# Kernel tuning notes

Hardware: AMD Instinct MI355X
Metric: run time of the kernel (lower is better)

Reference implementation:

```python
import math
import jax, jax.numpy as jnp
import numpy as np

N_HEAD = 4
D_MODEL = 96
BS, N_TOK = 32, 512
A2LEN = 150          # a2len % 16 != 0 so padn > 0 (asserted in torch code)
DST_MXLEN = 32


def setup_inputs() -> dict:
    key = jax.random.key(0)
    k1, k2, k3, k4, k5, k6 = jax.random.split(key, 6)
    x = jax.random.normal(k1, (BS, N_TOK, D_MODEL), dtype=jnp.float32)
    # LinearM: w is [outdim, indim+1], last column is the bias, zeroed at init
    wqv_w = 0.02 * jax.random.normal(k2, (3 * D_MODEL, D_MODEL + 1), dtype=jnp.float32)
    wqv_w = wqv_w.at[:, -1].set(0.0)
    fanout_w = 0.02 * jax.random.normal(k3, (D_MODEL, D_MODEL + 1), dtype=jnp.float32)
    fanout_w = fanout_w.at[:, -1].set(0.0)

    def make_coo(k):
        # COO triples [dst, src, dst_cnt]; every dst has DST_MXLEN sources
        dst = jnp.repeat(jnp.arange(N_TOK), DST_MXLEN)
        src = jax.random.randint(k, (N_TOK * DST_MXLEN,), 0, N_TOK)
        cnt = jnp.tile(jnp.arange(DST_MXLEN), N_TOK)
        return jnp.stack([dst, src, cnt], axis=1).astype(jnp.int32)

    coo0 = make_coo(k4)
    coo1 = make_coo(k5)
    a2a = jnp.sort(jax.random.permutation(k6, N_TOK)[:A2LEN]).astype(jnp.int32)
    return {"x": x, "wqv_w": wqv_w, "fanout_w": fanout_w,
            "coo0": coo0, "coo1": coo1, "a2a": a2a, "dst_mxlen": DST_MXLEN}


def _linm(w, x):
    # LinearM: einsum('oi,bhi->bho') + bias column
    return jnp.einsum('oi,bti->bto', w[:, :-1], x) + w[:, -1]


def _l1attn_sparse(v, q, k, coo, dst_mxlen):
    # l1attn_sparse_cuda.L1AttnSparse: per-(dst,src) L1 scores scattered into a
    # [n_tok, dst_mxlen] ragged table (pad = -1e12), softmax over the fan-in slot.
    bs, n_tok, h, w = q.shape
    dst, src, cnt = coo[:, 0], coo[:, 1], coo[:, 2]
    scale = 1.0 / math.sqrt(w)
    ww = -jnp.sum(jnp.abs(q[:, dst] - k[:, src]), axis=-1) * scale    # [bs, cl, h]
    attn = jnp.full((bs, n_tok, dst_mxlen, h), -1e12, dtype=q.dtype)
    attn = attn.at[:, dst, cnt, :].set(ww)
    attn_sm = jax.nn.softmax(attn, axis=2)
    vw = jnp.zeros((bs, n_tok, dst_mxlen, h, w), dtype=q.dtype)
    vw = vw.at[:, dst, cnt, :, :].set(v[:, src])                      # gather by src
    return jnp.einsum('bdrh,bdrhw->bdhw', attn_sm, vw)


def _forward(x, wqv_w, fanout_w, coo0, coo1, a2a, dst_mxlen):
    bs, n_tok, width = x.shape
    h = N_HEAD
    y = _linm(wqv_w, x)
    q, k, v = jnp.split(y, 3, axis=-1)

    # --- dense all-to-all L1 attention on tokens a2a, channels 72:96 (h*6) ---
    a2len = a2a.shape[0]
    q1 = q[:, a2a, 72:].reshape(bs, a2len, h, 6)
    k1 = k[:, a2a, 72:].reshape(bs, a2len, h, 6)
    v1 = v[:, a2a, 72:].reshape(bs, a2len, h, 6)
    padl = (a2len + 15) // 16 * 16
    q2 = jnp.pad(q1, ((0, 0), (0, padl - a2len), (0, 0), (0, 0)))
    k2 = jnp.pad(k1, ((0, 0), (0, padl - a2len), (0, 0), (0, 0)))
    scale = 1.0 / math.sqrt(6)
    # l1attn_cuda.L1Attn: a[b, s, d, h] = -scale * sum_w |q[b,d,h,w] - k[b,s,h,w]|
    a = -jnp.sum(jnp.abs(q2[:, None, :, :, :] - k2[:, :, None, :, :]), axis=-1) * scale
    a = a[:, :a2len + 1, :a2len + 1, :]   # keep one zero-score pad row (attention sink)
    a = jax.nn.softmax(a, axis=1)         # softmax over src dim
    a = a[:, :a2len, :a2len, :]
    b1 = jnp.einsum('bsdh,bshw->bdhw', a, v1)
    b2 = jnp.zeros((bs, n_tok, h, 6), dtype=x.dtype).at[:, a2a].set(b1)
    dense = b2.reshape(bs, n_tok, h * 6)

    # --- two sparse COO L1-attention groups: channels 32:52 and 52:72 (h*5) ---
    sparse_out = []
    for i, coo in enumerate((coo0, coo1)):
        sta = 32 + 20 * i
        q1 = q[:, :, sta:sta + 20].reshape(bs, n_tok, h, 5)
        k1 = k[:, :, sta:sta + 20].reshape(bs, n_tok, h, 5)
        v1 = v[:, :, sta:sta + 20].reshape(bs, n_tok, h, 5)
        sparse_out.append(_l1attn_sparse(v1, q1, k1, coo, dst_mxlen).reshape(bs, n_tok, h * 5))

    # channels 0:32 are never written -> zeros
    b = jnp.concatenate([jnp.zeros((bs, n_tok, 32), dtype=x.dtype),
                         sparse_out[0], sparse_out[1], dense], axis=-1)
    yb = b * jax.nn.sigmoid(1.702 * b)    # QuickGELU
    return x + _linm(fanout_w, yb)


def reference(x, wqv_w, fanout_w, coo0, coo1, a2a, dst_mxlen):
    return _forward(x, wqv_w, fanout_w, coo0, coo1, a2a, dst_mxlen)
```

## Files before the change

### kernel.cpp

```cpp
#include <hip/hip_runtime.h>
#include <hip/hip_bf16.h>
#include <math.h>

#define BS   32
#define T    512
#define BT   (BS * T)
#define D    96
#define H    4
#define MX   32
#define A2MAX 160

#define QKV_TOK  8
#define FUSE_TOK 8
#define DT       32

__global__ void transpose_kernel(const float* __restrict__ wqv,
                                 const float* __restrict__ fw,
                                 float* __restrict__ WT, float* __restrict__ FWT) {
    int idx = blockIdx.x * blockDim.x + threadIdx.x;
    if (idx < 97 * 192) {
        const int i = idx / 192, oc = idx - 192 * i;
        const int p = oc >> 6, c = oc & 63;
        WT[idx] = wqv[(p * 96 + 32 + c) * 97 + i];
    }
    idx -= 97 * 192;
    if (idx >= 0 && idx < 65 * 96) {
        const int i = idx / 96, o = idx - 96 * i;
        FWT[idx] = fw[o * 97 + 32 + i];
    }
}

__global__ void qkv_kernel(const float* __restrict__ x, const float* __restrict__ WT,
                           float* __restrict__ Q, float* __restrict__ K,
                           float* __restrict__ V) {
    const int tid  = threadIdx.x;
    const int base = blockIdx.x * QKV_TOK;
    __shared__ float xs[QKV_TOK * D];
    #pragma unroll
    for (int j = 0; j < 4; ++j) xs[tid + 192 * j] = x[base * D + tid + 192 * j];
    __syncthreads();
    float acc[QKV_TOK];
    const float bias = WT[96 * 192 + tid];
    #pragma unroll
    for (int j = 0; j < QKV_TOK; ++j) acc[j] = bias;
    #pragma unroll 4
    for (int i = 0; i < D; ++i) {
        const float wv = WT[i * 192 + tid];
        #pragma unroll
        for (int j = 0; j < QKV_TOK; ++j) acc[j] += wv * xs[j * D + i];
    }
    const int part = tid >> 6, c = tid & 63;
    float* out = (part == 0) ? Q : (part == 1 ? K : V);
    #pragma unroll
    for (int j = 0; j < QKV_TOK; ++j) out[(base + j) * 64 + c] = acc[j];
}

__global__ void scatter_kernel(const int* __restrict__ coo0,
                               const int* __restrict__ coo1,
                               int* __restrict__ srcs, int nedges) {
    const int id = blockIdx.x * blockDim.x + threadIdx.x;
    if (id >= 2 * nedges) return;
    const int ci = id / nedges;
    const int e  = id - ci * nedges;
    const int* row = (ci == 0 ? coo0 : coo1) + e * 3;
    const int dst = row[0], src = row[1], cnt = row[2];
    if (dst >= 0 && dst < T && cnt >= 0 && cnt < MX)
        srcs[(ci * T + dst) * MX + cnt] = src;
}

__global__ void sparse_kernel(const float* __restrict__ Q, const float* __restrict__ K,
                              const float* __restrict__ V, const int* __restrict__ srcs,
                              float* __restrict__ B) {
    const int b   = blockIdx.y;
    const int ci  = blockIdx.x >> 2, h = blockIdx.x & 3;
    const int base = 20 * ci + h * 5;
    const int tid  = threadIdx.x;
    __shared__ float ks[T * 8];
    __shared__ float vs[T * 8];
    for (int i = tid; i < T * 5; i += 256) {
        const int s = i / 5, w = i - 5 * s;
        const int g = (b * T + s) * 64 + base + w;
        ks[s * 8 + w] = K[g];
        vs[s * 8 + w] = V[g];
    }
    __syncthreads();
    const float iscale = 0.4472135954999579f;
    for (int t = tid; t < T; t += 256) {
        const int* sp   = srcs + (ci * T + t) * MX;
        const float* qp = Q + (b * T + t) * 64 + base;
        const float q0 = qp[0], q1 = qp[1], q2 = qp[2], q3 = qp[3], q4 = qp[4];
        float l = 0.f, o0 = 0.f, o1 = 0.f, o2 = 0.f, o3 = 0.f, o4 = 0.f;
        #pragma unroll 4
        for (int c = 0; c < MX; ++c) {
            const int s = sp[c];
            if (s < 0) continue;
            const float4 k4 = *(const float4*)&ks[s * 8];
            const float  k5 = ks[s * 8 + 4];
            const float sum = fabsf(q0 - k4.x) + fabsf(q1 - k4.y) +
                              fabsf(q2 - k4.z) + fabsf(q3 - k4.w) + fabsf(q4 - k5);
            const float e = __expf(-sum * iscale);
            const float4 v4 = *(const float4*)&vs[s * 8];
            const float  v5 = vs[s * 8 + 4];
            l  += e;
            o0 += e * v4.x; o1 += e * v4.y; o2 += e * v4.z;
            o3 += e * v4.w; o4 += e * v5;
        }
        const float inv = (l > 0.f) ? 1.f / l : 0.f;
        float* bp = B + (b * T + t) * 96 + 32 + base;
        bp[0] = o0 * inv; bp[1] = o1 * inv; bp[2] = o2 * inv;
        bp[3] = o3 * inv; bp[4] = o4 * inv;
    }
}

__global__ void dense_kernel(const float* __restrict__ Q, const float* __restrict__ K,
                             const float* __restrict__ V, const int* __restrict__ a2a,
                             int a2len, int extra, float* __restrict__ B) {
    const int b   = blockIdx.y;
    const int d0  = blockIdx.x * DT;
    const int tid = threadIdx.x;
    __shared__ int   rows[A2MAX];
    __shared__ float ks[A2MAX * 32];
    __shared__ float vs[A2MAX * 32];
    for (int i = tid; i < a2len; i += 128) rows[i] = a2a[i];
    __syncthreads();
    for (int i = tid; i < a2len * 24; i += 128) {
        const int s = i / 24, w = i - 24 * s;
        const int hh = w / 6, ww = w - 6 * hh;
        const int g = (b * T + rows[s]) * 64 + 40 + w;
        ks[s * 32 + hh * 8 + ww] = K[g];
        vs[s * 32 + hh * 8 + ww] = V[g];
    }
    __syncthreads();
    const int h = tid & 3, dl = tid >> 2;
    const int d = d0 + dl;
    if (d >= a2len) return;
    const int td = rows[d];
    const float scale = 0.4082482904638631f;
    const float* qp = Q + (b * T + td) * 64 + 40 + h * 6;
    const float q0 = qp[0], q1 = qp[1], q2 = qp[2],
                q3 = qp[3], q4 = qp[4], q5 = qp[5];
    float l = 0.f, o0 = 0.f, o1 = 0.f, o2 = 0.f, o3 = 0.f, o4 = 0.f, o5 = 0.f;
    for (int s = 0; s < a2len; ++s) {
        const float4 k4 = *(const float4*)&ks[s * 32 + h * 8];
        const float2 k2 = *(const float2*)&ks[s * 32 + h * 8 + 4];
        const float sum = fabsf(q0 - k4.x) + fabsf(q1 - k4.y) + fabsf(q2 - k4.z) +
                          fabsf(q3 - k4.w) + fabsf(q4 - k2.x) + fabsf(q5 - k2.y);
        const float e = __expf(-sum * scale);
        const float4 v4 = *(const float4*)&vs[s * 32 + h * 8];
        const float2 v2 = *(const float2*)&vs[s * 32 + h * 8 + 4];
        l  += e;
        o0 += e * v4.x; o1 += e * v4.y; o2 += e * v4.z;
        o3 += e * v4.w; o4 += e * v2.x; o5 += e * v2.y;
    }
    if (extra) {
        const float sum = fabsf(q0) + fabsf(q1) + fabsf(q2) +
                          fabsf(q3) + fabsf(q4) + fabsf(q5);
        l += __expf(-sum * scale);
    }
    const float inv = 1.f / l;
    float* bp = B + (b * T + td) * 96 + 72 + h * 6;
    bp[0] = o0 * inv; bp[1] = o1 * inv; bp[2] = o2 * inv;
    bp[3] = o3 * inv; bp[4] = o4 * inv; bp[5] = o5 * inv;
}

__global__ void fuse_kernel(const float* __restrict__ x, const float* __restrict__ FWT,
                            const float* __restrict__ B, float* __restrict__ out) {
    const int tid  = threadIdx.x;
    const int half = tid / 96;
    const int o    = tid - 96 * half;
    const int base = blockIdx.x * FUSE_TOK;
    __shared__ float yb[FUSE_TOK * 64];
    for (int idx = tid; idx < FUSE_TOK * 64; idx += 192) {
        const int j = idx >> 6, k = idx & 63;
        const float v = B[(base + j) * 96 + 32 + k];
        yb[idx] = v / (1.f + __expf(-1.702f * v));
    }
    __syncthreads();
    float acc[FUSE_TOK / 2];
    const float bias = FWT[64 * 96 + o];
    #pragma unroll
    for (int j = 0; j < FUSE_TOK / 2; ++j) acc[j] = bias;
    #pragma unroll 4
    for (int i = 0; i < 64; ++i) {
        const float wv = FWT[i * 96 + o];
        #pragma unroll
        for (int j = 0; j < FUSE_TOK / 2; ++j) acc[j] += wv * yb[(2 * j + half) * 64 + i];
    }
    #pragma unroll
    for (int j = 0; j < FUSE_TOK / 2; ++j) {
        const int token = base + 2 * j + half;
        out[token * D + o] = x[token * D + o] + acc[j];
    }
}

extern "C" void kernel_launch(void* const* d_in, const int* in_sizes, int n_in,
                              void* d_out, int out_size, void* d_ws, size_t ws_size,
                              hipStream_t stream) {
    const float* x   = (const float*)d_in[0];
    const float* wqv = (const float*)d_in[1];
    const float* fw  = (const float*)d_in[2];
    const int*  coo0 = (const int*)d_in[3];
    const int*  coo1 = (const int*)d_in[4];
    const int*  a2a  = (const int*)d_in[5];
    int a2len        = in_sizes[5];
    if (a2len > A2MAX) a2len = A2MAX;
    const int nedges = in_sizes[3] / 3;

    float* Q   = (float*)d_ws;
    float* K   = Q + (size_t)BT * 64;
    float* V   = K + (size_t)BT * 64;
    float* Bb  = V + (size_t)BT * 64;
    int*  srcs = (int*)(Bb + (size_t)BT * 96);
    float* WT  = (float*)(srcs + 2 * T * MX);
    float* FWT = WT + 97 * 192;

    hipMemsetAsync(srcs, 0xFF, 2 * T * MX * sizeof(int), stream);
    hipMemsetAsync(Bb, 0, (size_t)BT * 96 * sizeof(float), stream);

    transpose_kernel<<<(97 * 192 + 65 * 96 + 255) / 256, 256, 0, stream>>>(wqv, fw, WT, FWT);
    qkv_kernel<<<BT / QKV_TOK, 192, 0, stream>>>(x, WT, Q, K, V);
    scatter_kernel<<<(2 * nedges + 255) / 256, 256, 0, stream>>>(coo0, coo1, srcs, nedges);
    sparse_kernel<<<dim3(8, BS), 256, 0, stream>>>(Q, K, V, srcs, Bb);
    const int padl  = (a2len + 15) / 16 * 16;
    const int extra = (padl > a2len) ? 1 : 0;
    dense_kernel<<<dim3((a2len + DT - 1) / DT, BS), 128, 0, stream>>>(Q, K, V, a2a, a2len, extra, Bb);
    fuse_kernel<<<BT / FUSE_TOK, 192, 0, stream>>>(x, FWT, Bb, (float*)d_out);
}
```

Before: 145.0 us.

## Merge prep kernels, compact dense K/V, drop B memset, widen tiles

Folds the weight transposes, COO scatter and an a2a position flag into one prep kernel. The QKV projection also writes a compacted per-batch K/V copy for the dense-attention rows, so the dense kernel reads them contiguously with float4 loads instead of gathering. The large memset of B is removed and the fuse kernel zeroes the unwritten dense channels using the flag. Other changes: the sparse kernel stores K/V in struct-of-arrays shared memory and is split across a z grid dimension for more blocks, and the token tiles in the QKV and fuse GEMMs are doubled with float4 shared-memory reads. The cost is extra workspace, more registers per thread in the GEMMs, and bank conflicts from the scattered per-channel shared-memory reads in the sparse kernel.

Result: no change. 144.1 us (-0.6%).

```diff
diff --git a/kernel.cpp b/kernel.cpp
--- a/kernel.cpp
+++ b/kernel.cpp
@@ -2,70 +2,92 @@
 #include <hip/hip_bf16.h>
 #include <math.h>
 
-#define BS   32
-#define T    512
-#define BT   (BS * T)
-#define D    96
-#define H    4
-#define MX   32
+#define BS    32
+#define T     512
+#define BT    (BS * T)
+#define D     96
+#define H     4
+#define MX    32
 #define A2MAX 160
 
-#define QKV_TOK  8
-#define FUSE_TOK 8
+#define QKV_TOK  16
+#define FUSE_TOK 16
 #define DT       32
 
-__global__ void transpose_kernel(const float* __restrict__ wqv,
-                                 const float* __restrict__ fw,
-                                 float* __restrict__ WT, float* __restrict__ FWT) {
+__global__ void prep_kernel(const float* __restrict__ wqv, const float* __restrict__ fw,
+                            const int* __restrict__ coo0, const int* __restrict__ coo1,
+                            const int* __restrict__ a2a, int nedges, int a2len,
+                            float* __restrict__ WT, float* __restrict__ FWT,
+                            int* __restrict__ srcs, int* __restrict__ flag) {
     int idx = blockIdx.x * blockDim.x + threadIdx.x;
     if (idx < 97 * 192) {
         const int i = idx / 192, oc = idx - 192 * i;
         const int p = oc >> 6, c = oc & 63;
         WT[idx] = wqv[(p * 96 + 32 + c) * 97 + i];
+        return;
     }
     idx -= 97 * 192;
-    if (idx >= 0 && idx < 65 * 96) {
+    if (idx < 65 * 96) {
         const int i = idx / 96, o = idx - 96 * i;
         FWT[idx] = fw[o * 97 + 32 + i];
-    }
+        return;
+    }
+    idx -= 65 * 96;
+    if (idx < 2 * nedges) {
+        const int ci = idx / nedges;
+        const int e  = idx - ci * nedges;
+        const int* row = (ci == 0 ? coo0 : coo1) + e * 3;
+        const int dst = row[0], src = row[1], cnt = row[2];
+        if (dst >= 0 && dst < T && cnt >= 0 && cnt < MX)
+            srcs[(ci * T + dst) * MX + cnt] = src;
+        return;
+    }
+    idx -= 2 * nedges;
+    if (idx < a2len) flag[a2a[idx]] = idx;
 }
 
 __global__ void qkv_kernel(const float* __restrict__ x, const float* __restrict__ WT,
+                           const int* __restrict__ flag,
                            float* __restrict__ Q, float* __restrict__ K,
-                           float* __restrict__ V) {
+                           float* __restrict__ V,
+                           float* __restrict__ Kg, float* __restrict__ Vg) {
     const int tid  = threadIdx.x;
     const int base = blockIdx.x * QKV_TOK;
     __shared__ float xs[QKV_TOK * D];
-    #pragma unroll
-    for (int j = 0; j < 4; ++j) xs[tid + 192 * j] = x[base * D + tid + 192 * j];
+    float4* xs4 = (float4*)xs;
+    const float4* xg = (const float4*)(x + base * D);
+    xs4[tid]       = xg[tid];
+    xs4[tid + 192] = xg[tid + 192];
     __syncthreads();
     float acc[QKV_TOK];
     const float bias = WT[96 * 192 + tid];
     #pragma unroll
     for (int j = 0; j < QKV_TOK; ++j) acc[j] = bias;
-    #pragma unroll 4
-    for (int i = 0; i < D; ++i) {
-        const float wv = WT[i * 192 + tid];
-        #pragma unroll
-        for (int j = 0; j < QKV_TOK; ++j) acc[j] += wv * xs[j * D + i];
+    #pragma unroll 3
+    for (int i4 = 0; i4 < 24; ++i4) {
+        const float w0 = WT[(4 * i4 + 0) * 192 + tid];
+        const float w1 = WT[(4 * i4 + 1) * 192 + tid];
+        const float w2 = WT[(4 * i4 + 2) * 192 + tid];
+        const float w3 = WT[(4 * i4 + 3) * 192 + tid];
+        #pragma unroll
+        for (int j = 0; j < QKV_TOK; ++j) {
+            const float4 xv = xs4[j * 24 + i4];
+            acc[j] += w0 * xv.x + w1 * xv.y + w2 * xv.z + w3 * xv.w;
+        }
     }
     const int part = tid >> 6, c = tid & 63;
     float* out = (part == 0) ? Q : (part == 1 ? K : V);
     #pragma unroll
     for (int j = 0; j < QKV_TOK; ++j) out[(base + j) * 64 + c] = acc[j];
-}
-
-__global__ void scatter_kernel(const int* __restrict__ coo0,
-                               const int* __restrict__ coo1,
-                               int* __restrict__ srcs, int nedges) {
-    const int id = blockIdx.x * blockDim.x + threadIdx.x;
-    if (id >= 2 * nedges) return;
-    const int ci = id / nedges;
-    const int e  = id - ci * nedges;
-    const int* row = (ci == 0 ? coo0 : coo1) + e * 3;
-    const int dst = row[0], src = row[1], cnt = row[2];
-    if (dst >= 0 && dst < T && cnt >= 0 && cnt < MX)
-        srcs[(ci * T + dst) * MX + cnt] = src;
+    if (part >= 1 && c >= 40) {
+        float* g = (part == 1) ? Kg : Vg;
+        const int b = base >> 9;
+        #pragma unroll
+        for (int j = 0; j < QKV_TOK; ++j) {
+            const int ps = flag[(base + j) & (T - 1)];
+            if (ps >= 0) g[(b * A2MAX + ps) * 24 + (c - 40)] = acc[j];
+        }
+    }
 }
 
 __global__ void sparse_kernel(const float* __restrict__ Q, const float* __restrict__ K,
@@ -75,45 +97,48 @@
     const int ci  = blockIdx.x >> 2, h = blockIdx.x & 3;
     const int base = 20 * ci + h * 5;
     const int tid  = threadIdx.x;
-    __shared__ float ks[T * 8];
-    __shared__ float vs[T * 8];
-    for (int i = tid; i < T * 5; i += 256) {
-        const int s = i / 5, w = i - 5 * s;
+    __shared__ float ks[5 * T];
+    __shared__ float vs[5 * T];
+    for (int i = tid; i < 5 * T; i += 256) {
+        const int s = i & (T - 1), w = i >> 9;
         const int g = (b * T + s) * 64 + base + w;
-        ks[s * 8 + w] = K[g];
-        vs[s * 8 + w] = V[g];
+        ks[w * T + s] = K[g];
+        vs[w * T + s] = V[g];
     }
     __syncthreads();
     const float iscale = 0.4472135954999579f;
-    for (int t = tid; t < T; t += 256) {
-        const int* sp   = srcs + (ci * T + t) * MX;
-        const float* qp = Q + (b * T + t) * 64 + base;
-        const float q0 = qp[0], q1 = qp[1], q2 = qp[2], q3 = qp[3], q4 = qp[4];
-        float l = 0.f, o0 = 0.f, o1 = 0.f, o2 = 0.f, o3 = 0.f, o4 = 0.f;
-        #pragma unroll 4
-        for (int c = 0; c < MX; ++c) {
-            const int s = sp[c];
+    const int t = blockIdx.z * 256 + tid;
+    const int4* sp4 = (const int4*)(srcs + (ci * T + t) * MX);
+    const float* qp = Q + (b * T + t) * 64 + base;
+    const float q0 = qp[0], q1 = qp[1], q2 = qp[2], q3 = qp[3], q4 = qp[4];
+    float l = 0.f, o0 = 0.f, o1 = 0.f, o2 = 0.f, o3 = 0.f, o4 = 0.f;
+    #pragma unroll 2
+    for (int c4 = 0; c4 < MX / 4; ++c4) {
+        const int4 s4 = sp4[c4];
+        const int sv[4] = {s4.x, s4.y, s4.z, s4.w};
+        #pragma unroll
+        for (int m = 0; m < 4; ++m) {
+            const int s = sv[m];
             if (s < 0) continue;
-            const float4 k4 = *(const float4*)&ks[s * 8];
-            const float  k5 = ks[s * 8 + 4];
-            const float sum = fabsf(q0 - k4.x) + fabsf(q1 - k4.y) +
-                              fabsf(q2 - k4.z) + fabsf(q3 - k4.w) + fabsf(q4 - k5);
+            const float sum = fabsf(q0 - ks[s]) + fabsf(q1 - ks[T + s]) +
+                              fabsf(q2 - ks[2 * T + s]) + fabsf(q3 - ks[3 * T + s]) +
+                              fabsf(q4 - ks[4 * T + s]);
             const float e = __expf(-sum * iscale);
-            const float4 v4 = *(const float4*)&vs[s * 8];
-            const float  v5 = vs[s * 8 + 4];
             l  += e;
-            o0 += e * v4.x; o1 += e * v4.y; o2 += e * v4.z;
-            o3 += e * v4.w; o4 += e * v5;
-        }
-        const float inv = (l > 0.f) ? 1.f / l : 0.f;
-        float* bp = B + (b * T + t) * 96 + 32 + base;
-        bp[0] = o0 * inv; bp[1] = o1 * inv; bp[2] = o2 * inv;
-        bp[3] = o3 * inv; bp[4] = o4 * inv;
-    }
-}
-
-__global__ void dense_kernel(const float* __restrict__ Q, const float* __restrict__ K,
-                             const float* __restrict__ V, const int* __restrict__ a2a,
+            o0 += e * vs[s];         o1 += e * vs[T + s];
+            o2 += e * vs[2 * T + s]; o3 += e * vs[3 * T + s];
+            o4 += e * vs[4 * T + s];
+        }
+    }
+    const float inv = (l > 0.f) ? 1.f / l : 0.f;
+    float* bp = B + (b * T + t) * 96 + 32 + base;
+    bp[0] = o0 * inv; bp[1] = o1 * inv; bp[2] = o2 * inv;
+    bp[3] = o3 * inv; bp[4] = o4 * inv;
+}
+
+__global__ void dense_kernel(const float* __restrict__ Q,
+                             const float* __restrict__ Kg, const float* __restrict__ Vg,
+                             const int* __restrict__ a2a,
                              int a2len, int extra, float* __restrict__ B) {
     const int b   = blockIdx.y;
     const int d0  = blockIdx.x * DT;
@@ -122,13 +147,21 @@
     __shared__ float ks[A2MAX * 32];
     __shared__ float vs[A2MAX * 32];
     for (int i = tid; i < a2len; i += 128) rows[i] = a2a[i];
-    __syncthreads();
-    for (int i = tid; i < a2len * 24; i += 128) {
-        const int s = i / 24, w = i - 24 * s;
-        const int hh = w / 6, ww = w - 6 * hh;
-        const int g = (b * T + rows[s]) * 64 + 40 + w;
-        ks[s * 32 + hh * 8 + ww] = K[g];
-        vs[s * 32 + hh * 8 + ww] = V[g];
+    const int nq = (a2len * 24) / 4;
+    const float4* kg4 = (const float4*)(Kg + (size_t)b * A2MAX * 24);
+    const float4* vg4 = (const float4*)(Vg + (size_t)b * A2MAX * 24);
+    for (int idx = tid; idx < nq; idx += 128) {
+        const int s = idx / 6, r = idx - 6 * s;
+        const float4 kk = kg4[idx];
+        const float4 vv = vg4[idx];
+        const float kv[4] = {kk.x, kk.y, kk.z, kk.w};
+        const float vv4[4] = {vv.x, vv.y, vv.z, vv.w};
+        #pragma unroll
+        for (int m = 0; m < 4; ++m) {
+            const int w = r * 4 + m, hh = w / 6, ww = w - 6 * hh;
+            ks[s * 32 + hh * 8 + ww] = kv[m];
+            vs[s * 32 + hh * 8 + ww] = vv4[m];
+        }
     }
     __syncthreads();
     const int h = tid & 3, dl = tid >> 2;
@@ -164,15 +197,18 @@
 }
 
 __global__ void fuse_kernel(const float* __restrict__ x, const float* __restrict__ FWT,
-                            const float* __restrict__ B, float* __restrict__ out) {
+                            const float* __restrict__ B, const int* __restrict__ flag,
+                            float* __restrict__ out) {
     const int tid  = threadIdx.x;
     const int half = tid / 96;
     const int o    = tid - 96 * half;
     const int base = blockIdx.x * FUSE_TOK;
     __shared__ float yb[FUSE_TOK * 64];
+    float4* yb4 = (float4*)yb;
     for (int idx = tid; idx < FUSE_TOK * 64; idx += 192) {
         const int j = idx >> 6, k = idx & 63;
-        const float v = B[(base + j) * 96 + 32 + k];
+        float v = B[(base + j) * 96 + 32 + k];
+        if (k >= 40 && flag[(base + j) & (T - 1)] < 0) v = 0.f;
         yb[idx] = v / (1.f + __expf(-1.702f * v));
     }
     __syncthreads();
@@ -180,11 +216,17 @@
     const float bias = FWT[64 * 96 + o];
     #pragma unroll
     for (int j = 0; j < FUSE_TOK / 2; ++j) acc[j] = bias;
-    #pragma unroll 4
-    for (int i = 0; i < 64; ++i) {
-        const float wv = FWT[i * 96 + o];
-        #pragma unroll
-        for (int j = 0; j < FUSE_TOK / 2; ++j) acc[j] += wv * yb[(2 * j + half) * 64 + i];
+    #pragma unroll 2
+    for (int i4 = 0; i4 < 16; ++i4) {
+        const float w0 = FWT[(4 * i4 + 0) * 96 + o];
+        const float w1 = FWT[(4 * i4 + 1) * 96 + o];
+        const float w2 = FWT[(4 * i4 + 2) * 96 + o];
+        const float w3 = FWT[(4 * i4 + 3) * 96 + o];
+        #pragma unroll
+        for (int j = 0; j < FUSE_TOK / 2; ++j) {
+            const float4 yv = yb4[(2 * j + half) * 16 + i4];
+            acc[j] += w0 * yv.x + w1 * yv.y + w2 * yv.z + w3 * yv.w;
+        }
     }
     #pragma unroll
     for (int j = 0; j < FUSE_TOK / 2; ++j) {
@@ -207,22 +249,26 @@
     const int nedges = in_sizes[3] / 3;
 
     float* Q   = (float*)d_ws;
-    float* K   = Q + (size_t)BT * 64;
-    float* V   = K + (size_t)BT * 64;
-    float* Bb  = V + (size_t)BT * 64;
-    int*  srcs = (int*)(Bb + (size_t)BT * 96);
-    float* WT  = (float*)(srcs + 2 * T * MX);
+    float* K   = Q  + (size_t)BT * 64;
+    float* V   = K  + (size_t)BT * 64;
+    float* Bb  = V  + (size_t)BT * 64;
+    float* Kg  = Bb + (size_t)BT * 96;
+    float* Vg  = Kg + (size_t)BS * A2MAX * 24;
+    int*  srcs = (int*)(Vg + (size_t)BS * A2MAX * 24);
+    int*  flag = srcs + 2 * T * MX;
+    float* WT  = (float*)(flag + T);
     float* FWT = WT + 97 * 192;
 
-    hipMemsetAsync(srcs, 0xFF, 2 * T * MX * sizeof(int), stream);
-    hipMemsetAsync(Bb, 0, (size_t)BT * 96 * sizeof(float), stream);
-
-    transpose_kernel<<<(97 * 192 + 65 * 96 + 255) / 256, 256, 0, stream>>>(wqv, fw, WT, FWT);
-    qkv_kernel<<<BT / QKV_TOK, 192, 0, stream>>>(x, WT, Q, K, V);
-    scatter_kernel<<<(2 * nedges + 255) / 256, 256, 0, stream>>>(coo0, coo1, srcs, nedges);
-    sparse_kernel<<<dim3(8, BS), 256, 0, stream>>>(Q, K, V, srcs, Bb);
+    hipMemsetAsync(srcs, 0xFF, (2 * T * MX + T) * sizeof(int), stream);
+
+    const int prep_n = 97 * 192 + 65 * 96 + 2 * nedges + a2len;
+    prep_kernel<<<(prep_n + 255) / 256, 256, 0, stream>>>(
+        wqv, fw, coo0, coo1, a2a, nedges, a2len, WT, FWT, srcs, flag);
+    qkv_kernel<<<BT / QKV_TOK, 192, 0, stream>>>(x, WT, flag, Q, K, V, Kg, Vg);
+    sparse_kernel<<<dim3(8, BS, 2), 256, 0, stream>>>(Q, K, V, srcs, Bb);
     const int padl  = (a2len + 15) / 16 * 16;
     const int extra = (padl > a2len) ? 1 : 0;
-    dense_kernel<<<dim3((a2len + DT - 1) / DT, BS), 128, 0, stream>>>(Q, K, V, a2a, a2len, extra, Bb);
-    fuse_kernel<<<BT / FUSE_TOK, 192, 0, stream>>>(x, FWT, Bb, (float*)d_out);
-}
+    dense_kernel<<<dim3((a2len + DT - 1) / DT, BS), 128, 0, stream>>>(
+        Q, Kg, Vg, a2a, a2len, extra, Bb);
+    fuse_kernel<<<BT / FUSE_TOK, 192, 0, stream>>>(x, FWT, Bb, flag, (float*)d_out);
+}
```
